# Optimization experiments

Hardware: AMD Instinct MI355X
Metric: run time of the kernel (lower is better)

Reference implementation:

```python
import jax, jax.numpy as jnp
import numpy as np

T, B, L, CTX, H = 512, 512, 16, 64, 128
STATE_DIM, SHOT, PID, DATA = 32, 12, 35, 23


def setup_inputs() -> dict:
    key = jax.random.key(0)
    ks = jax.random.split(key, 64)
    k = iter(ks)
    def rn(shape, s=0.1):
        return (jax.random.normal(next(k), shape) * s).astype(jnp.float32)
    xs = jax.random.normal(next(k), (T, B, DATA), jnp.float32)
    xs = xs.at[:, :, 12].set(jax.random.randint(next(k), (T, B), 0, SHOT).astype(jnp.float32))
    xs = xs.at[:, :, 17].set(jax.random.randint(next(k), (T, B), 0, PID).astype(jnp.float32))
    xs = xs.at[:, :, 20].set(jax.random.randint(next(k), (T, B), 0, SHOT).astype(jnp.float32))
    return dict(
        total_xs=jnp.zeros((1,), jnp.float32),
        xs=xs,
        ts=jnp.linspace(0.0, 2.0, T).astype(jnp.float32),
        noise_std=jnp.asarray(0.1, jnp.float32),
        z0_noise=jax.random.normal(next(k), (B, L), jnp.float32),
        bm_noise=jax.random.normal(next(k), (T - 1, B, L), jnp.float32),
        shot_emb=rn((SHOT, 8)), player_emb=rn((PID, 8)),
        gru_wih=rn((3 * H, STATE_DIM)), gru_whh=rn((3 * H, H)),
        gru_bih=rn((3 * H,)), gru_bhh=rn((3 * H,)),
        enc_w=rn((CTX, H)), enc_b=rn((CTX,)),
        qz0_w=rn((2 * L, CTX)), qz0_b=rn((2 * L,)),
        f_w1=rn((H, L + CTX)), f_b1=rn((H,)), f_w2=rn((H, H)), f_b2=rn((H,)),
        f_w3=rn((L, H)), f_b3=rn((L,)),
        h_w1=rn((H, L)), h_b1=rn((H,)), h_w2=rn((H, H)), h_b2=rn((H,)),
        h_w3=rn((L, H)), h_b3=rn((L,)),
        g_w1=rn((L, H)), g_b1=rn((L, H)), g_w2=rn((L, H)), g_b2=rn((L,)),
        proj_w=rn((STATE_DIM, L)), proj_b=rn((STATE_DIM,)),
        pz0_mean=jnp.zeros((1, L), jnp.float32), pz0_logstd=jnp.zeros((1, L), jnp.float32),
        act_w=rn((128, L)), act_b=rn((128,)),
        act_land_w=rn((2, 128)), act_shot_w=rn((SHOT, 128)), act_move_w=rn((2, 128)),
    )


def _forward(xs, noise_std, shot_emb, player_emb, gru_wih, gru_whh, gru_bih, gru_bhh,
             enc_w, enc_b, qz0_w, qz0_b,
             f_w1, f_b1, f_w2, f_b2, f_w3, f_b3,
             h_w1, h_b1, h_w2, h_b2, h_w3, h_b3,
             g_w1, g_b1, g_w2, g_b2,
             proj_w, proj_b, pz0_mean, pz0_logstd,
             act_w, act_b, act_land_w, act_shot_w, act_move_w,
             ts, z0_noise, bm_noise):
    # --- SDE_embed_and_transform: replace shot/player id cols with embeddings ---
    state = xs[:, :, :18]
    shot_ids = state[:, :, 12].astype(jnp.int32)
    pid_ids = state[:, :, 17].astype(jnp.int32)
    state_t = jnp.concatenate([state[:, :, :12], shot_emb[shot_ids],
                               state[:, :, 13:17], player_emb[pid_ids]], axis=-1)  # (T,B,32)
    xs_t = jnp.concatenate([state_t, xs[:, :, 18:]], axis=-1)  # (T,B,37)
    # --- Encoder: GRU over time-reversed states, linear head, flip back ---
    def gru_step(h, xt):
        gi = xt @ gru_wih.T + gru_bih
        gh = h @ gru_whh.T + gru_bhh
        ir, iz, inn = jnp.split(gi, 3, axis=-1)
        hr, hz, hn = jnp.split(gh, 3, axis=-1)
        r = jax.nn.sigmoid(ir + hr)
        zg = jax.nn.sigmoid(iz + hz)
        n = jnp.tanh(inn + r * hn)
        hnew = (1.0 - zg) * n + zg * h
        return hnew, hnew
    h0 = jnp.zeros((xs.shape[1], gru_whh.shape[1]), xs.dtype)
    _, hs = jax.lax.scan(gru_step, h0, state_t[::-1])
    ctx = (hs @ enc_w.T + enc_b)[::-1]  # (T,B,CTX)
    # --- posterior z0 ---
    qm, qls = jnp.split(ctx[0] @ qz0_w.T + qz0_b, 2, axis=1)
    z0 = qm + jnp.exp(qls) * z0_noise
    # --- Euler-Maruyama with logqp; searchsorted(right) -> ctx[min(i+1,T-1)] = ctx[i+1] ---
    dts = ts[1:] - ts[:-1]  # (T-1,)
    dW = jnp.sqrt(dts)[:, None, None] * bm_noise
    ctx_steps = ctx[1:]
    def mlp3(x, w1, b1, w2, b2, w3, b3):
        h1 = jax.nn.softplus(x @ w1.T + b1)
        h2 = jax.nn.softplus(h1 @ w2.T + b2)
        return h2 @ w3.T + b3
    def g_diag(y):  # (B,L): per-latent-dim scalar nets, batched over L
        hg = jax.nn.softplus(y[:, :, None] * g_w1[None] + g_b1[None])  # (B,L,H)
        return jax.nn.sigmoid(jnp.einsum('blh,lh->bl', hg, g_w2) + g_b2)
    def sde_step(z, inp):
        c, dw, dt = inp
        f_val = mlp3(jnp.concatenate([z, c], axis=1), f_w1, f_b1, f_w2, f_b2, f_w3, f_b3)
        h_val = mlp3(z, h_w1, h_b1, h_w2, h_b2, h_w3, h_b3)
        g_val = g_diag(z)
        u = (f_val - h_val) / g_val
        logr = 0.5 * jnp.sum(u * u, axis=1) * dt
        z_new = z + f_val * dt + g_val * dw
        return z_new, (z_new, logr)
    _, (z_tail, log_ratio) = jax.lax.scan(sde_step, z0, (ctx_steps, dW, dts))
    zs = jnp.concatenate([z0[None], z_tail], axis=0)  # (T,B,L)
    _xs = zs @ proj_w.T + proj_b  # (T,B,32)
    # --- action model losses ---
    a = jax.nn.relu(zs @ act_w.T + act_b)
    land = (a @ act_land_w.T).reshape(-1, 2)
    shot_logits = (a @ act_shot_w.T).reshape(-1, act_shot_w.shape[0])
    move = (a @ act_move_w.T).reshape(-1, 2)
    true_actions = xs_t[:, :, -5:]
    true_land = true_actions[:, :, :2].reshape(-1, 2)
    true_move = true_actions[:, :, 3:].reshape(-1, 2)
    true_shot = true_actions[:, :, 2].astype(jnp.int32).reshape(-1)
    land_loss = jnp.mean((land - true_land) ** 2)
    move_loss = jnp.mean((move - true_move) ** 2)
    logp = jax.nn.log_softmax(shot_logits, axis=-1)
    picked = jnp.take_along_axis(logp, true_shot[:, None], axis=1)[:, 0]
    mask = (true_shot != 0).astype(logp.dtype)  # CrossEntropy ignore_index=0
    shot_loss = -jnp.sum(picked * mask) / jnp.maximum(jnp.sum(mask), 1.0)
    # --- reconstruction log-likelihood ---
    xs_state = xs_t[:, :, :STATE_DIM]
    LOG2PI = 1.8378770664093453
    log_pxs = jnp.mean(jnp.sum(
        -0.5 * ((xs_state - _xs) / noise_std) ** 2 - jnp.log(noise_std) - 0.5 * LOG2PI,
        axis=(0, 2)))
    # --- KL(q(z0) || p(z0)) ---
    var_q = jnp.exp(2.0 * qls)
    var_p = jnp.exp(2.0 * pz0_logstd)
    kl = pz0_logstd - qls + (var_q + (qm - pz0_mean) ** 2) / (2.0 * var_p) - 0.5
    logqp0 = jnp.mean(jnp.sum(kl, axis=1))
    logqp_path = jnp.mean(jnp.sum(log_ratio, axis=0))
    return log_pxs, logqp0 + logqp_path + land_loss + shot_loss + move_loss


def reference(total_xs, xs, ts, noise_std, z0_noise, bm_noise, shot_emb, player_emb,
              gru_wih, gru_whh, gru_bih, gru_bhh, enc_w, enc_b, qz0_w, qz0_b,
              f_w1, f_b1, f_w2, f_b2, f_w3, f_b3, h_w1, h_b1, h_w2, h_b2, h_w3, h_b3,
              g_w1, g_b1, g_w2, g_b2, proj_w, proj_b, pz0_mean, pz0_logstd,
              act_w, act_b, act_land_w, act_shot_w, act_move_w):
    return _forward(xs, noise_std, shot_emb, player_emb, gru_wih, gru_whh, gru_bih, gru_bhh,
                    enc_w, enc_b, qz0_w, qz0_b,
                    f_w1, f_b1, f_w2, f_b2, f_w3, f_b3,
                    h_w1, h_b1, h_w2, h_b2, h_w3, h_b3,
                    g_w1, g_b1, g_w2, g_b2,
                    proj_w, proj_b, pz0_mean, pz0_logstd,
                    act_w, act_b, act_land_w, act_shot_w, act_move_w,
                    ts, z0_noise, bm_noise)
```

## Files before the change

kernel.cpp:

```cpp
#include <hip/hip_runtime.h>
#include <cstdint>

typedef _Float16 f16;
typedef _Float16 f16x2 __attribute__((ext_vector_type(2)));

#define T_STEPS 512
#define B_SZ 512
#define LOG2PI 1.8378770664093453f

__device__ __forceinline__ uint32_t packh2(float a, float b) {
  f16x2 v; v[0] = (f16)a; v[1] = (f16)b;
  return __builtin_bit_cast(uint32_t, v);
}

__device__ __forceinline__ float fdot2(uint32_t a, uint32_t b, float c) {
#if defined(__AMDGCN__) && __has_builtin(__builtin_amdgcn_fdot2)
  return __builtin_amdgcn_fdot2(__builtin_bit_cast(f16x2, a),
                                __builtin_bit_cast(f16x2, b), c, false);
#else
  f16x2 x = __builtin_bit_cast(f16x2, a), y = __builtin_bit_cast(f16x2, b);
  return c + (float)x[0] * (float)y[0] + (float)x[1] * (float)y[1];
#endif
}

#define DOT4(acc, w0, w1, w2, w3, v)                                     \
  do {                                                                   \
    acc = fdot2((w0), (v).x, acc); acc = fdot2((w1), (v).y, acc);        \
    acc = fdot2((w2), (v).z, acc); acc = fdot2((w3), (v).w, acc);        \
  } while (0)

__device__ __forceinline__ float sigmoidf_(float x) {
  return 1.0f / (1.0f + __expf(-x));
}
__device__ __forceinline__ float tanhf_(float x) {
  float ax = fabsf(x);
  float t = __expf(-2.0f * ax);
  float r = (1.0f - t) / (1.0f + t);
  return copysignf(r, x);
}
__device__ __forceinline__ float softplusf_(float x) {
  return fmaxf(x, 0.0f) + __logf(1.0f + __expf(-fabsf(x)));
}

__global__ __launch_bounds__(256) void k_embed(
    const float* __restrict__ xs, const float* __restrict__ shot_emb,
    const float* __restrict__ player_emb, f16* __restrict__ state_t,
    float* __restrict__ accums) {
  if (blockIdx.x == 0 && threadIdx.x < 16) accums[threadIdx.x] = 0.0f;
  size_t idx = (size_t)blockIdx.x * 256 + threadIdx.x;
  const float* xp = xs + idx * 23;
  f16* op = state_t + idx * 32;
  int sid = (int)xp[12];
  int pid = (int)xp[17];
#pragma unroll
  for (int i = 0; i < 12; ++i) op[i] = (f16)xp[i];
  const float* se = shot_emb + sid * 8;
#pragma unroll
  for (int i = 0; i < 8; ++i) op[12 + i] = (f16)se[i];
#pragma unroll
  for (int i = 0; i < 4; ++i) op[20 + i] = (f16)xp[13 + i];
  const float* pe = player_emb + pid * 8;
#pragma unroll
  for (int i = 0; i < 8; ++i) op[24 + i] = (f16)pe[i];
}

__global__ __launch_bounds__(512) void k_gru(
    const f16* __restrict__ state_t, const float* __restrict__ wih,
    const float* __restrict__ whh, const float* __restrict__ bih,
    const float* __restrict__ bhh, const float* __restrict__ enc_w,
    const float* __restrict__ enc_b, const float* __restrict__ qz0_w,
    const float* __restrict__ qz0_b, const float* __restrict__ z0_noise,
    const float* __restrict__ pz0_mean, const float* __restrict__ pz0_logstd,
    f16* __restrict__ ctx, float* __restrict__ z0_out,
    float* __restrict__ accums) {
  __shared__ uint32_t s_x[2][16];
  __shared__ uint32_t s_h[2][64];
  __shared__ float s_gates[2 * 128 * 4];
  __shared__ float s_encp[2 * 64 * 2];
  __shared__ float s_ctx0[2][64];
  __shared__ float s_q[2][32];

  const int tid = threadIdx.x;
  const int bbase = blockIdx.x * 2;
  const uint32_t* stu = (const uint32_t*)state_t;

  uint32_t wA[64];
  uint32_t wB[16];
  float bias0 = 0.f, bias1 = 0.f, encbr = 0.f;

  if (tid < 256) {
    int g = tid >> 7, du = tid & 127;
    const float* whr = whh + (size_t)(g * 128 + du) * 128;
#pragma unroll
    for (int i = 0; i < 64; ++i) wA[i] = packh2(whr[2 * i], whr[2 * i + 1]);
    const float* wxr = wih + (size_t)(g * 128 + du) * 32;
#pragma unroll
    for (int i = 0; i < 16; ++i) wB[i] = packh2(wxr[2 * i], wxr[2 * i + 1]);
    bias0 = bih[g * 128 + du] + bhh[g * 128 + du];
  } else if (tid < 384) {
    int du = tid - 256;
    const float* whr = whh + (size_t)(256 + du) * 128;
#pragma unroll
    for (int i = 0; i < 64; ++i) wA[i] = packh2(whr[2 * i], whr[2 * i + 1]);
    const float* wxr = wih + (size_t)(256 + du) * 32;
#pragma unroll
    for (int i = 0; i < 16; ++i) wB[i] = packh2(wxr[2 * i], wxr[2 * i + 1]);
    bias0 = bih[256 + du];
    bias1 = bhh[256 + du];
  } else {
    int e = tid - 384, c = e & 63, ks = e >> 6;
    const float* wer = enc_w + (size_t)c * 128 + ks * 64;
#pragma unroll
    for (int i = 0; i < 32; ++i) wA[i] = packh2(wer[2 * i], wer[2 * i + 1]);
    encbr = enc_b[c];
  }

  if (tid < 128) s_h[tid >> 6][tid & 63] = 0u;
  if (tid < 32) {
    int b = tid >> 4, i = tid & 15;
    s_x[b][i] = stu[((size_t)(T_STEPS - 1) * B_SZ + bbase + b) * 16 + i];
  }
  float h_old = 0.0f;
  __syncthreads();

  for (int t = T_STEPS - 1; t >= 0; --t) {
    uint4 xpref = make_uint4(0, 0, 0, 0);
    if (tid < 256) {
      int g = tid >> 7, du = tid & 127;
#pragma unroll
      for (int b = 0; b < 2; ++b) {
        float a = bias0;
        const uint4* xq = (const uint4*)&s_x[b][0];
#pragma unroll
        for (int j = 0; j < 4; ++j) {
          uint4 v = xq[j];
          DOT4(a, wB[4 * j], wB[4 * j + 1], wB[4 * j + 2], wB[4 * j + 3], v);
        }
        const uint4* hq = (const uint4*)&s_h[b][0];
#pragma unroll
        for (int j = 0; j < 16; ++j) {
          uint4 v = hq[j];
          DOT4(a, wA[4 * j], wA[4 * j + 1], wA[4 * j + 2], wA[4 * j + 3], v);
        }
        s_gates[(b * 128 + du) * 4 + g] = a;
      }
    } else if (tid < 384) {
      int du = tid - 256;
#pragma unroll
      for (int b = 0; b < 2; ++b) {
        float aI = bias0, aH = bias1;
        const uint4* xq = (const uint4*)&s_x[b][0];
#pragma unroll
        for (int j = 0; j < 4; ++j) {
          uint4 v = xq[j];
          DOT4(aI, wB[4 * j], wB[4 * j + 1], wB[4 * j + 2], wB[4 * j + 3], v);
        }
        const uint4* hq = (const uint4*)&s_h[b][0];
#pragma unroll
        for (int j = 0; j < 16; ++j) {
          uint4 v = hq[j];
          DOT4(aH, wA[4 * j], wA[4 * j + 1], wA[4 * j + 2], wA[4 * j + 3], v);
        }
        s_gates[(b * 128 + du) * 4 + 2] = aI;
        s_gates[(b * 128 + du) * 4 + 3] = aH;
      }
    } else {
      int e = tid - 384, ks = e >> 6, cc = e & 63;
      (void)cc;
      if (t < T_STEPS - 1) {
#pragma unroll
        for (int b = 0; b < 2; ++b) {
          float a = 0.f;
          const uint4* hq = (const uint4*)&s_h[b][ks * 32];
#pragma unroll
          for (int j = 0; j < 8; ++j) {
            uint4 v = hq[j];
            DOT4(a, wA[4 * j], wA[4 * j + 1], wA[4 * j + 2], wA[4 * j + 3], v);
          }
          s_encp[(b * 64 + cc) * 2 + ks] = a;
        }
      }
      if (e < 8 && t > 0) {
        int b = e & 1, q = e >> 1;
        xpref = *(const uint4*)(stu +
                                ((size_t)(t - 1) * B_SZ + bbase + b) * 16 + q * 4);
      }
    }
    __syncthreads();
    if (tid < 256) {
      int b = tid >> 7, du = tid & 127;
      const float4 gt = *(const float4*)&s_gates[(b * 128 + du) * 4];
      float r = sigmoidf_(gt.x), zg = sigmoidf_(gt.y);
      float n = tanhf_(gt.z + r * gt.w);
      float hnew = (1.0f - zg) * n + zg * h_old;
      h_old = hnew;
      ((f16*)&s_h[b][0])[du] = (f16)hnew;
    } else if (tid >= 384) {
      int e = tid - 384, cc = e & 63, b = e >> 6;
      if (t < T_STEPS - 1) {
        float2 p = *(const float2*)&s_encp[(b * 64 + cc) * 2];
        ctx[((size_t)(t + 1) * B_SZ + bbase + b) * 64 + cc] =
            (f16)(p.x + p.y + encbr);
      }
      if (e < 8 && t > 0) {
        int b2 = e & 1, q = e >> 1;
        *(uint4*)&s_x[b2][q * 4] = xpref;
      }
    }
    __syncthreads();
  }

  if (tid >= 384) {
    int e = tid - 384, ks = e >> 6, cc = e & 63;
#pragma unroll
    for (int b = 0; b < 2; ++b) {
      float a = 0.f;
      const uint4* hq = (const uint4*)&s_h[b][ks * 32];
#pragma unroll
      for (int j = 0; j < 8; ++j) {
        uint4 v = hq[j];
        DOT4(a, wA[4 * j], wA[4 * j + 1], wA[4 * j + 2], wA[4 * j + 3], v);
      }
      s_encp[(b * 64 + cc) * 2 + ks] = a;
    }
  }
  __syncthreads();
  if (tid >= 384) {
    int e = tid - 384, cc = e & 63, b = e >> 6;
    float2 p = *(const float2*)&s_encp[(b * 64 + cc) * 2];
    float val = p.x + p.y + encbr;
    ctx[((size_t)bbase + b) * 64 + cc] = (f16)val;
    s_ctx0[b][cc] = val;
  }
  __syncthreads();
  if (tid < 64) {
    int b = tid >> 5, o = tid & 31;
    float acc = qz0_b[o];
#pragma unroll 8
    for (int k = 0; k < 64; ++k) acc += qz0_w[o * 64 + k] * s_ctx0[b][k];
    s_q[b][o] = acc;
  }
  __syncthreads();
  if (tid < 32) {
    int b = tid >> 4, l = tid & 15;
    int bg = bbase + b;
    float qm = s_q[b][l], qls = s_q[b][16 + l];
    float z0v = qm + __expf(qls) * z0_noise[bg * 16 + l];
    z0_out[bg * 16 + l] = z0v;
    float pm = pz0_mean[l], pls = pz0_logstd[l];
    float var_q = __expf(2.0f * qls);
    float var_p = __expf(2.0f * pls);
    float dm = qm - pm;
    float kl = pls - qls + (var_q + dm * dm) / (2.0f * var_p) - 0.5f;
    atomicAdd(&accums[5], kl);
  }
}

__global__ __launch_bounds__(512) void k_sde(
    const f16* __restrict__ ctx, const float* __restrict__ z0_in,
    const float* __restrict__ ts, const float* __restrict__ bm_noise,
    const float* __restrict__ fw1, const float* __restrict__ fb1,
    const float* __restrict__ fw2, const float* __restrict__ fb2,
    const float* __restrict__ fw3, const float* __restrict__ fb3,
    const float* __restrict__ hw1, const float* __restrict__ hb1,
    const float* __restrict__ hw2, const float* __restrict__ hb2,
    const float* __restrict__ hw3, const float* __restrict__ hb3,
    const float* __restrict__ gw1, const float* __restrict__ gb1,
    const float* __restrict__ gw2, const float* __restrict__ gb2,
    f16* __restrict__ zs, float* __restrict__ accums) {
  __shared__ uint32_t s_x2[2][40];
  __shared__ float s_zf[2][16];
  __shared__ uint32_t s_h1[2][2][64];
  __shared__ uint32_t s_h2[2][2][64];
  __shared__ float s_gp[256];
  __shared__ float s_gv[32];
  __shared__ float s_p2[2 * 2 * 128 * 2];
  __shared__ float s_p3[2 * 2 * 16 * 8];
  __shared__ float s_dts[512];

  const int tid = threadIdx.x;
  const int bbase = blockIdx.x * 2;

  uint32_t uw[48];
  uint32_t wP2[32];
  uint32_t wP3[8];
  float bias1r = 0.f, bias2r = 0.f, gb2r = 0.f, fb3r = 0.f, hb3r = 0.f;

  if (tid < 256) {
    int l = tid & 15, k8 = (tid >> 4) & 7;
#pragma unroll
    for (int i = 0; i < 16; ++i) {
      int h = k8 * 16 + i;
      uw[i] = __builtin_bit_cast(uint32_t, gw1[l * 128 + h]);
      uw[16 + i] = __builtin_bit_cast(uint32_t, gb1[l * 128 + h]);
      uw[32 + i] = __builtin_bit_cast(uint32_t, gw2[l * 128 + h]);
    }
  } else if (tid < 384) {
    int u = tid - 256;
    const float* w = fw1 + (size_t)u * 80;
#pragma unroll
    for (int i = 0; i < 40; ++i) uw[i] = packh2(w[2 * i], w[2 * i + 1]);
    bias1r = fb1[u];
  } else {
    int u = tid - 384;
    const float* w = hw1 + (size_t)u * 16;
#pragma unroll
    for (int i = 0; i < 8; ++i) uw[i] = packh2(w[2 * i], w[2 * i + 1]);
    bias1r = hb1[u];
  }
  {
    int u = tid & 127, ks = (tid >> 7) & 1, mlp = tid >> 8;
    const float* w = (mlp ? hw2 : fw2) + (size_t)u * 128 + ks * 64;
#pragma unroll
    for (int i = 0; i < 32; ++i) wP2[i] = packh2(w[2 * i], w[2 * i + 1]);
    bias2r = (mlp ? hb2 : fb2)[u];
  }
  if (tid < 128 || (tid >= 256 && tid < 384)) {
    int o = tid & 15, k8 = (tid >> 4) & 7;
    const float* w = ((tid >= 256) ? hw3 : fw3) + (size_t)o * 128 + k8 * 16;
#pragma unroll
    for (int i = 0; i < 8; ++i) wP3[i] = packh2(w[2 * i], w[2 * i + 1]);
  }
  if (tid >= 128 && tid < 160) gb2r = gb2[tid & 15];
  if (tid < 32) {
    fb3r = fb3[tid & 15];
    hb3r = hb3[tid & 15];
  }

  if (tid < 511) s_dts[tid] = ts[tid + 1] - ts[tid];
  float bmc = 0.f;
  uint4 cpref = make_uint4(0, 0, 0, 0);
  if (tid < 32) {
    int b = tid >> 4, l = tid & 15, bg = bbase + b;
    float z = z0_in[bg * 16 + l];
    s_zf[b][l] = z;
    ((f16*)&s_x2[b][0])[l] = (f16)z;
    zs[(size_t)bg * 16 + l] = (f16)z;
    bmc = bm_noise[((size_t)0 * B_SZ + bg) * 16 + l];
  }
  if (tid >= 32 && tid < 48) {
    int i = tid - 32, b = i & 1, q = i >> 1;
    const uint32_t* cu = (const uint32_t*)ctx;
    uint4 v = *(const uint4*)(cu + ((size_t)1 * B_SZ + bbase + b) * 32 + q * 4);
    *(uint4*)&s_x2[b][8 + q * 4] = v;
  }
  float path_acc = 0.0f;
  __syncthreads();

  for (int t = 0; t < T_STEPS - 1; ++t) {
    float bmn = 0.f;
    if (tid < 32 && t < T_STEPS - 2) {
      int b = tid >> 4, l = tid & 15, bg = bbase + b;
      bmn = bm_noise[((size_t)(t + 1) * B_SZ + bg) * 16 + l];
    }
    if (tid >= 32 && tid < 48 && t <= T_STEPS - 3) {
      int i = tid - 32, b = i & 1, q = i >> 1;
      const uint32_t* cu = (const uint32_t*)ctx;
      cpref = *(const uint4*)(cu +
                              ((size_t)(t + 2) * B_SZ + bbase + b) * 32 + q * 4);
    }
    if (tid < 256) {
      int b = tid >> 7, l = tid & 15, k8 = (tid >> 4) & 7;
      float y = s_zf[b][l];
      float acc = 0.f;
#pragma unroll
      for (int i = 0; i < 16; ++i) {
        float pre = fmaf(y, __builtin_bit_cast(float, uw[i]),
                         __builtin_bit_cast(float, uw[16 + i]));
        acc = fmaf(softplusf_(pre), __builtin_bit_cast(float, uw[32 + i]), acc);
      }
      s_gp[(b * 16 + l) * 8 + k8] = acc;
    } else if (tid < 384) {
      int u = tid - 256;
#pragma unroll
      for (int b = 0; b < 2; ++b) {
        float a = bias1r;
        const uint4* xq = (const uint4*)&s_x2[b][0];
#pragma unroll
        for (int j = 0; j < 10; ++j) {
          uint4 v = xq[j];
          DOT4(a, uw[4 * j], uw[4 * j + 1], uw[4 * j + 2], uw[4 * j + 3], v);
        }
        ((f16*)&s_h1[0][b][0])[u] = (f16)softplusf_(a);
      }
    } else {
      int u = tid - 384;
#pragma unroll
      for (int b = 0; b < 2; ++b) {
        float a = bias1r;
        const uint4* xq = (const uint4*)&s_x2[b][0];
#pragma unroll
        for (int j = 0; j < 2; ++j) {
          uint4 v = xq[j];
          DOT4(a, uw[4 * j], uw[4 * j + 1], uw[4 * j + 2], uw[4 * j + 3], v);
        }
        ((f16*)&s_h1[1][b][0])[u] = (f16)softplusf_(a);
      }
    }
    __syncthreads();
    {
      int u = tid & 127, ks = (tid >> 7) & 1, mlp = tid >> 8;
#pragma unroll
      for (int b = 0; b < 2; ++b) {
        float a = 0.f;
        const uint4* hq = (const uint4*)&s_h1[mlp][b][ks * 32];
#pragma unroll
        for (int j = 0; j < 8; ++j) {
          uint4 v = hq[j];
          DOT4(a, wP2[4 * j], wP2[4 * j + 1], wP2[4 * j + 2], wP2[4 * j + 3], v);
        }
        s_p2[((mlp * 2 + b) * 128 + u) * 2 + ks] = a;
      }
    }
    __syncthreads();
    {
      int u = tid & 127, b = (tid >> 7) & 1, mlp = tid >> 8;
      float2 p = *(const float2*)&s_p2[((mlp * 2 + b) * 128 + u) * 2];
      ((f16*)&s_h2[mlp][b][0])[u] = (f16)softplusf_(p.x + p.y + bias2r);
    }
    __syncthreads();
    if (tid < 128 || (tid >= 256 && tid < 384)) {
      int o = tid & 15, k8 = (tid >> 4) & 7, mlp = tid >> 8;
#pragma unroll
      for (int b = 0; b < 2; ++b) {
        float a = 0.f;
        const uint4* hq = (const uint4*)&s_h2[mlp][b][k8 * 8];
#pragma unroll
        for (int j = 0; j < 2; ++j) {
          uint4 v = hq[j];
          DOT4(a, wP3[4 * j], wP3[4 * j + 1], wP3[4 * j + 2], wP3[4 * j + 3], v);
        }
        s_p3[((mlp * 2 + b) * 16 + o) * 8 + k8] = a;
      }
    } else if (tid >= 128 && tid < 160) {
      int i = tid - 128, b = i >> 4, l = i & 15;
      const float4* gp = (const float4*)&s_gp[(b * 16 + l) * 8];
      float4 g0 = gp[0], g1 = gp[1];
      float sum = g0.x + g0.y + g0.z + g0.w + g1.x + g1.y + g1.z + g1.w + gb2r;
      s_gv[b * 16 + l] = sigmoidf_(sum);
    }
    __syncthreads();
    if (tid < 32) {
      int b = tid >> 4, l = tid & 15, bg = bbase + b;
      const float4* fp = (const float4*)&s_p3[((0 * 2 + b) * 16 + l) * 8];
      const float4* hp = (const float4*)&s_p3[((2 + b) * 16 + l) * 8];
      float4 f0 = fp[0], f1v = fp[1], h0 = hp[0], h1v = hp[1];
      float fv = fb3r + f0.x + f0.y + f0.z + f0.w + f1v.x + f1v.y + f1v.z + f1v.w;
      float hv = hb3r + h0.x + h0.y + h0.z + h0.w + h1v.x + h1v.y + h1v.z + h1v.w;
      float gv = s_gv[b * 16 + l];
      float dt = s_dts[t];
      float u = (fv - hv) / gv;
      float lsum = u * u;
      lsum += __shfl_xor(lsum, 1);
      lsum += __shfl_xor(lsum, 2);
      lsum += __shfl_xor(lsum, 4);
      lsum += __shfl_xor(lsum, 8);
      if (l == 0) path_acc += 0.5f * lsum * dt;
      float dw = sqrtf(dt) * bmc;
      float zn = s_zf[b][l] + fv * dt + gv * dw;
      s_zf[b][l] = zn;
      ((f16*)&s_x2[b][0])[l] = (f16)zn;
      zs[((size_t)(t + 1) * B_SZ + bg) * 16 + l] = (f16)zn;
      bmc = bmn;
    } else if (tid >= 32 && tid < 48 && t <= T_STEPS - 3) {
      int i = tid - 32, b = i & 1, q = i >> 1;
      *(uint4*)&s_x2[b][8 + q * 4] = cpref;
    }
    __syncthreads();
  }
  if (tid < 32 && (tid & 15) == 0) atomicAdd(&accums[6], path_acc);
}

__global__ __launch_bounds__(256) void k_dec(
    const f16* __restrict__ zs, const f16* __restrict__ state_t,
    const float* __restrict__ xs, const float* __restrict__ proj_w,
    const float* __restrict__ proj_b, const float* __restrict__ act_w,
    const float* __restrict__ act_b, const float* __restrict__ land_w,
    const float* __restrict__ shot_w, const float* __restrict__ move_w,
    float* __restrict__ accums) {
  __shared__ uint32_t s_proj[8 * 32];
  __shared__ uint32_t s_act[8 * 128];
  __shared__ uint32_t s_head[128 * 8];
  __shared__ float s_pb[32], s_ab[128];
  __shared__ float s_red[4 * 5];

  const int tid = threadIdx.x;
  for (int id = tid; id < 8 * 32; id += 256) {
    int kp = id & 7, n = id >> 3;
    s_proj[kp * 32 + n] = packh2(proj_w[n * 16 + 2 * kp], proj_w[n * 16 + 2 * kp + 1]);
  }
  for (int id = tid; id < 8 * 128; id += 256) {
    int kp = id & 7, n = id >> 3;
    s_act[kp * 128 + n] = packh2(act_w[n * 16 + 2 * kp], act_w[n * 16 + 2 * kp + 1]);
  }
  for (int id = tid; id < 128 * 8; id += 256) {
    int j = id >> 3, p = id & 7;
    int h0 = 2 * p, h1 = 2 * p + 1;
    float w0 = (h0 < 2) ? land_w[h0 * 128 + j]
                        : (h0 < 14 ? shot_w[(h0 - 2) * 128 + j]
                                   : move_w[(h0 - 14) * 128 + j]);
    float w1 = (h1 < 2) ? land_w[h1 * 128 + j]
                        : (h1 < 14 ? shot_w[(h1 - 2) * 128 + j]
                                   : move_w[(h1 - 14) * 128 + j]);
    s_head[j * 8 + p] = packh2(w0, w1);
  }
  if (tid < 32) s_pb[tid] = proj_b[tid];
  if (tid < 128) s_ab[tid] = act_b[tid];
  __syncthreads();

  size_t idx = (size_t)blockIdx.x * 256 + tid;
  uint32_t z2[8];
  const uint32_t* zp = (const uint32_t*)(zs + idx * 16);
#pragma unroll
  for (int i = 0; i < 8; ++i) z2[i] = zp[i];
  uint32_t stv[16];
  const uint32_t* stp = (const uint32_t*)(state_t + idx * 32);
#pragma unroll
  for (int i = 0; i < 16; ++i) stv[i] = stp[i];

  float sqsum = 0.0f;
#pragma unroll 4
  for (int i = 0; i < 32; ++i) {
    float acc = s_pb[i];
#pragma unroll
    for (int kp = 0; kp < 8; ++kp) acc = fdot2(s_proj[kp * 32 + i], z2[kp], acc);
    f16x2 sv = __builtin_bit_cast(f16x2, stv[i >> 1]);
    float d = (float)sv[i & 1] - acc;
    sqsum += d * d;
  }

  float hd[16];
#pragma unroll
  for (int i = 0; i < 16; ++i) hd[i] = 0.0f;
#pragma unroll 2
  for (int j = 0; j < 128; ++j) {
    float a = s_ab[j];
#pragma unroll
    for (int kp = 0; kp < 8; ++kp) a = fdot2(s_act[kp * 128 + j], z2[kp], a);
    a = fmaxf(a, 0.0f);
#pragma unroll
    for (int p = 0; p < 8; ++p) {
      f16x2 w = __builtin_bit_cast(f16x2, s_head[j * 8 + p]);
      hd[2 * p] += (float)w[0] * a;
      hd[2 * p + 1] += (float)w[1] * a;
    }
  }
  const float* xp = xs + idx * 23;
  float dl0 = hd[0] - xp[18], dl1 = hd[1] - xp[19];
  float land = dl0 * dl0 + dl1 * dl1;
  float dm0 = hd[14] - xp[21], dm1 = hd[15] - xp[22];
  float move = dm0 * dm0 + dm1 * dm1;
  int sid = (int)xp[20];
  float m = hd[2];
#pragma unroll
  for (int s = 1; s < 12; ++s) m = fmaxf(m, hd[2 + s]);
  float sume = 0.0f;
#pragma unroll
  for (int s = 0; s < 12; ++s) sume += __expf(hd[2 + s] - m);
  float lse = m + __logf(sume);
  float pl = 0.0f;
#pragma unroll
  for (int s = 0; s < 12; ++s)
    if (s == sid) pl = hd[2 + s];
  float picked = 0.0f, cnt = 0.0f;
  if (sid != 0) {
    picked = pl - lse;
    cnt = 1.0f;
  }
  float vals[5] = {sqsum, land, move, picked, cnt};
#pragma unroll
  for (int v = 0; v < 5; ++v) {
    float x = vals[v];
    for (int off = 1; off < 64; off <<= 1) x += __shfl_xor(x, off);
    vals[v] = x;
  }
  int lane = tid & 63, wv = tid >> 6;
  if (lane == 0) {
#pragma unroll
    for (int v = 0; v < 5; ++v) s_red[wv * 5 + v] = vals[v];
  }
  __syncthreads();
  if (tid == 0) {
#pragma unroll
    for (int v = 0; v < 5; ++v) {
      float s = s_red[v] + s_red[5 + v] + s_red[10 + v] + s_red[15 + v];
      atomicAdd(&accums[v], s);
    }
  }
}

__global__ void k_fin(const float* __restrict__ accums,
                      const float* __restrict__ noise_std,
                      float* __restrict__ out) {
  if (threadIdx.x == 0 && blockIdx.x == 0) {
    float sd = noise_std[0];
    float log_pxs = -0.5f * accums[0] / (sd * sd * (float)B_SZ) -
                    (float)T_STEPS * 32.0f * (logf(sd) + 0.5f * LOG2PI);
    float land = accums[1] / (float)(T_STEPS * B_SZ * 2);
    float move = accums[2] / (float)(T_STEPS * B_SZ * 2);
    float shot = -accums[3] / fmaxf(accums[4], 1.0f);
    float out1 = accums[5] / (float)B_SZ + accums[6] / (float)B_SZ + land + shot + move;
    out[0] = log_pxs;
    out[1] = out1;
  }
}

extern "C" void kernel_launch(void* const* d_in, const int* in_sizes, int n_in,
                              void* d_out, int out_size, void* d_ws,
                              size_t ws_size, hipStream_t stream) {
  const float* xs = (const float*)d_in[1];
  const float* ts = (const float*)d_in[2];
  const float* noise_std = (const float*)d_in[3];
  const float* z0_noise = (const float*)d_in[4];
  const float* bm_noise = (const float*)d_in[5];
  const float* shot_emb = (const float*)d_in[6];
  const float* player_emb = (const float*)d_in[7];
  const float* gru_wih = (const float*)d_in[8];
  const float* gru_whh = (const float*)d_in[9];
  const float* gru_bih = (const float*)d_in[10];
  const float* gru_bhh = (const float*)d_in[11];
  const float* enc_w = (const float*)d_in[12];
  const float* enc_b = (const float*)d_in[13];
  const float* qz0_w = (const float*)d_in[14];
  const float* qz0_b = (const float*)d_in[15];
  const float* f_w1 = (const float*)d_in[16];
  const float* f_b1 = (const float*)d_in[17];
  const float* f_w2 = (const float*)d_in[18];
  const float* f_b2 = (const float*)d_in[19];
  const float* f_w3 = (const float*)d_in[20];
  const float* f_b3 = (const float*)d_in[21];
  const float* h_w1 = (const float*)d_in[22];
  const float* h_b1 = (const float*)d_in[23];
  const float* h_w2 = (const float*)d_in[24];
  const float* h_b2 = (const float*)d_in[25];
  const float* h_w3 = (const float*)d_in[26];
  const float* h_b3 = (const float*)d_in[27];
  const float* g_w1 = (const float*)d_in[28];
  const float* g_b1 = (const float*)d_in[29];
  const float* g_w2 = (const float*)d_in[30];
  const float* g_b2 = (const float*)d_in[31];
  const float* proj_w = (const float*)d_in[32];
  const float* proj_b = (const float*)d_in[33];
  const float* pz0_mean = (const float*)d_in[34];
  const float* pz0_logstd = (const float*)d_in[35];
  const float* act_w = (const float*)d_in[36];
  const float* act_b = (const float*)d_in[37];
  const float* act_land_w = (const float*)d_in[38];
  const float* act_shot_w = (const float*)d_in[39];
  const float* act_move_w = (const float*)d_in[40];

  char* ws = (char*)d_ws;
  float* accums = (float*)ws;
  f16* state_t = (f16*)(ws + 256);
  f16* ctx = (f16*)(ws + 256 + 16777216);
  float* z0b = (float*)(ws + 256 + 16777216 + 33554432);
  f16* zs = (f16*)(ws + 256 + 16777216 + 33554432 + 32768);

  k_embed<<<1024, 256, 0, stream>>>(xs, shot_emb, player_emb, state_t, accums);
  k_gru<<<256, 512, 0, stream>>>(state_t, gru_wih, gru_whh, gru_bih, gru_bhh,
                                 enc_w, enc_b, qz0_w, qz0_b, z0_noise, pz0_mean,
                                 pz0_logstd, ctx, z0b, accums);
  k_sde<<<256, 512, 0, stream>>>(ctx, z0b, ts, bm_noise, f_w1, f_b1, f_w2, f_b2,
                                 f_w3, f_b3, h_w1, h_b1, h_w2, h_b2, h_w3, h_b3,
                                 g_w1, g_b1, g_w2, g_b2, zs, accums);
  k_dec<<<1024, 256, 0, stream>>>(zs, state_t, xs, proj_w, proj_b, act_w, act_b,
                                  act_land_w, act_shot_w, act_move_w, accums);
  k_fin<<<1, 64, 0, stream>>>(accums, noise_std, (float*)d_out);
}
```

Measured before the change: 1.996 ms.

## Reduce SDE step barriers via shuffle reductions and fused output-layer epilogue

Reassigns thread mappings in the per-timestep SDE loop so the split-K partial sums of the second layer are combined with lane shuffles instead of a shared-memory pass. The third layer and the drift/diffusion update are merged into one phase using shuffles, which removes the s_p2, s_p3 and s_gv buffers and two __syncthreads per step. Dot-product loops also gain split accumulators to shorten dependency chains. The cost is more registers per thread (larger wP3) and concentrating the final-layer work on 128 threads.

```diff
diff --git a/kernel.cpp b/kernel.cpp
--- a/kernel.cpp
+++ b/kernel.cpp
@@ -273,9 +273,6 @@
   __shared__ uint32_t s_h1[2][2][64];
   __shared__ uint32_t s_h2[2][2][64];
   __shared__ float s_gp[256];
-  __shared__ float s_gv[32];
-  __shared__ float s_p2[2 * 2 * 128 * 2];
-  __shared__ float s_p3[2 * 2 * 16 * 8];
   __shared__ float s_dts[512];
 
   const int tid = threadIdx.x;
@@ -283,7 +280,7 @@
 
   uint32_t uw[48];
   uint32_t wP2[32];
-  uint32_t wP3[8];
+  uint32_t wP3[32];
   float bias1r = 0.f, bias2r = 0.f, gb2r = 0.f, fb3r = 0.f, hb3r = 0.f;
 
   if (tid < 256) {
@@ -309,52 +306,52 @@
     bias1r = hb1[u];
   }
   {
-    int u = tid & 127, ks = (tid >> 7) & 1, mlp = tid >> 8;
+    int u = (tid >> 1) & 127, ks = tid & 1, mlp = tid >> 8;
     const float* w = (mlp ? hw2 : fw2) + (size_t)u * 128 + ks * 64;
 #pragma unroll
     for (int i = 0; i < 32; ++i) wP2[i] = packh2(w[2 * i], w[2 * i + 1]);
     bias2r = (mlp ? hb2 : fb2)[u];
   }
-  if (tid < 128 || (tid >= 256 && tid < 384)) {
-    int o = tid & 15, k8 = (tid >> 4) & 7;
-    const float* w = ((tid >= 256) ? hw3 : fw3) + (size_t)o * 128 + k8 * 16;
-#pragma unroll
-    for (int i = 0; i < 8; ++i) wP3[i] = packh2(w[2 * i], w[2 * i + 1]);
-  }
-  if (tid >= 128 && tid < 160) gb2r = gb2[tid & 15];
-  if (tid < 32) {
-    fb3r = fb3[tid & 15];
-    hb3r = hb3[tid & 15];
+  if (tid < 128) {
+    int l = (tid >> 2) & 15, mlp = (tid >> 1) & 1, kh = tid & 1;
+    const float* w = (mlp ? hw3 : fw3) + (size_t)l * 128 + kh * 64;
+#pragma unroll
+    for (int i = 0; i < 32; ++i) wP3[i] = packh2(w[2 * i], w[2 * i + 1]);
+    if ((tid & 3) == 0) {
+      gb2r = gb2[l];
+      fb3r = fb3[l];
+      hb3r = hb3[l];
+    }
   }
 
   if (tid < 511) s_dts[tid] = ts[tid + 1] - ts[tid];
   float bmc = 0.f;
+  float path_acc = 0.0f;
   uint4 cpref = make_uint4(0, 0, 0, 0);
-  if (tid < 32) {
-    int b = tid >> 4, l = tid & 15, bg = bbase + b;
+  if (tid < 128 && (tid & 3) == 0) {
+    int b = tid >> 6, l = (tid >> 2) & 15, bg = bbase + b;
     float z = z0_in[bg * 16 + l];
     s_zf[b][l] = z;
     ((f16*)&s_x2[b][0])[l] = (f16)z;
     zs[(size_t)bg * 16 + l] = (f16)z;
     bmc = bm_noise[((size_t)0 * B_SZ + bg) * 16 + l];
   }
-  if (tid >= 32 && tid < 48) {
-    int i = tid - 32, b = i & 1, q = i >> 1;
+  if (tid >= 128 && tid < 144) {
+    int i = tid - 128, b = i & 1, q = i >> 1;
     const uint32_t* cu = (const uint32_t*)ctx;
     uint4 v = *(const uint4*)(cu + ((size_t)1 * B_SZ + bbase + b) * 32 + q * 4);
     *(uint4*)&s_x2[b][8 + q * 4] = v;
   }
-  float path_acc = 0.0f;
   __syncthreads();
 
   for (int t = 0; t < T_STEPS - 1; ++t) {
     float bmn = 0.f;
-    if (tid < 32 && t < T_STEPS - 2) {
-      int b = tid >> 4, l = tid & 15, bg = bbase + b;
-      bmn = bm_noise[((size_t)(t + 1) * B_SZ + bg) * 16 + l];
-    }
-    if (tid >= 32 && tid < 48 && t <= T_STEPS - 3) {
-      int i = tid - 32, b = i & 1, q = i >> 1;
+    if (tid < 128 && (tid & 3) == 0 && t < T_STEPS - 2) {
+      int b = tid >> 6, l = (tid >> 2) & 15;
+      bmn = bm_noise[((size_t)(t + 1) * B_SZ + bbase + b) * 16 + l];
+    }
+    if (tid >= 128 && tid < 144 && t <= T_STEPS - 3) {
+      int i = tid - 128, b = i & 1, q = i >> 1;
       const uint32_t* cu = (const uint32_t*)ctx;
       cpref = *(const uint4*)(cu +
                               ((size_t)(t + 2) * B_SZ + bbase + b) * 32 + q * 4);
@@ -374,14 +371,15 @@
       int u = tid - 256;
 #pragma unroll
       for (int b = 0; b < 2; ++b) {
-        float a = bias1r;
+        float a0 = bias1r, a1 = 0.f;
         const uint4* xq = (const uint4*)&s_x2[b][0];
 #pragma unroll
-        for (int j = 0; j < 10; ++j) {
-          uint4 v = xq[j];
-          DOT4(a, uw[4 * j], uw[4 * j + 1], uw[4 * j + 2], uw[4 * j + 3], v);
+        for (int j = 0; j < 10; j += 2) {
+          uint4 v0 = xq[j], v1 = xq[j + 1];
+          DOT4(a0, uw[4 * j], uw[4 * j + 1], uw[4 * j + 2], uw[4 * j + 3], v0);
+          DOT4(a1, uw[4 * j + 4], uw[4 * j + 5], uw[4 * j + 6], uw[4 * j + 7], v1);
         }
-        ((f16*)&s_h1[0][b][0])[u] = (f16)softplusf_(a);
+        ((f16*)&s_h1[0][b][0])[u] = (f16)softplusf_(a0 + a1);
       }
     } else {
       int u = tid - 384;
@@ -399,76 +397,68 @@
     }
     __syncthreads();
     {
-      int u = tid & 127, ks = (tid >> 7) & 1, mlp = tid >> 8;
-#pragma unroll
-      for (int b = 0; b < 2; ++b) {
-        float a = 0.f;
-        const uint4* hq = (const uint4*)&s_h1[mlp][b][ks * 32];
-#pragma unroll
-        for (int j = 0; j < 8; ++j) {
-          uint4 v = hq[j];
-          DOT4(a, wP2[4 * j], wP2[4 * j + 1], wP2[4 * j + 2], wP2[4 * j + 3], v);
-        }
-        s_p2[((mlp * 2 + b) * 128 + u) * 2 + ks] = a;
-      }
+      int u = (tid >> 1) & 127, ks = tid & 1, mlp = tid >> 8;
+      float p0a = 0.f, p0b = 0.f, p1a = 0.f, p1b = 0.f;
+      const uint4* h0q = (const uint4*)&s_h1[mlp][0][ks * 32];
+      const uint4* h1q = (const uint4*)&s_h1[mlp][1][ks * 32];
+#pragma unroll
+      for (int j = 0; j < 8; j += 2) {
+        uint4 v0 = h0q[j], v1 = h0q[j + 1];
+        DOT4(p0a, wP2[4 * j], wP2[4 * j + 1], wP2[4 * j + 2], wP2[4 * j + 3], v0);
+        DOT4(p0b, wP2[4 * j + 4], wP2[4 * j + 5], wP2[4 * j + 6], wP2[4 * j + 7], v1);
+        uint4 w0 = h1q[j], w1 = h1q[j + 1];
+        DOT4(p1a, wP2[4 * j], wP2[4 * j + 1], wP2[4 * j + 2], wP2[4 * j + 3], w0);
+        DOT4(p1b, wP2[4 * j + 4], wP2[4 * j + 5], wP2[4 * j + 6], wP2[4 * j + 7], w1);
+      }
+      float p0 = p0a + p0b, p1 = p1a + p1b;
+      p0 += __shfl_xor(p0, 1);
+      p1 += __shfl_xor(p1, 1);
+      float sel = ks ? p1 : p0;
+      ((f16*)&s_h2[mlp][ks][0])[u] = (f16)softplusf_(sel + bias2r);
     }
     __syncthreads();
-    {
-      int u = tid & 127, b = (tid >> 7) & 1, mlp = tid >> 8;
-      float2 p = *(const float2*)&s_p2[((mlp * 2 + b) * 128 + u) * 2];
-      ((f16*)&s_h2[mlp][b][0])[u] = (f16)softplusf_(p.x + p.y + bias2r);
+    if (tid < 128) {
+      int b = tid >> 6, l = (tid >> 2) & 15, mlp = (tid >> 1) & 1, kh = tid & 1;
+      const uint4* hq = (const uint4*)&s_h2[mlp][b][kh * 32];
+      float a0 = 0.f, a1 = 0.f;
+#pragma unroll
+      for (int j = 0; j < 8; j += 2) {
+        uint4 v0 = hq[j], v1 = hq[j + 1];
+        DOT4(a0, wP3[4 * j], wP3[4 * j + 1], wP3[4 * j + 2], wP3[4 * j + 3], v0);
+        DOT4(a1, wP3[4 * j + 4], wP3[4 * j + 5], wP3[4 * j + 6], wP3[4 * j + 7], v1);
+      }
+      float a = a0 + a1;
+      float full = a + __shfl_xor(a, 1);
+      float other = __shfl_xor(full, 2);
+      if ((tid & 3) == 0) {
+        float fv = full + fb3r;
+        float hv = other + hb3r;
+        const float4* gp = (const float4*)&s_gp[(b * 16 + l) * 8];
+        float4 g0 = gp[0], g1 = gp[1];
+        float gv = sigmoidf_(g0.x + g0.y + g0.z + g0.w +
+                             g1.x + g1.y + g1.z + g1.w + gb2r);
+        float dt = s_dts[t];
+        float u_ = (fv - hv) / gv;
+        float lsum = u_ * u_;
+        lsum += __shfl_xor(lsum, 4);
+        lsum += __shfl_xor(lsum, 8);
+        lsum += __shfl_xor(lsum, 16);
+        lsum += __shfl_xor(lsum, 32);
+        if (l == 0) path_acc += 0.5f * lsum * dt;
+        float dw = sqrtf(dt) * bmc;
+        float zn = s_zf[b][l] + fv * dt + gv * dw;
+        s_zf[b][l] = zn;
+        ((f16*)&s_x2[b][0])[l] = (f16)zn;
+        zs[((size_t)(t + 1) * B_SZ + bbase + b) * 16 + l] = (f16)zn;
+        bmc = bmn;
+      }
+    } else if (tid >= 128 && tid < 144 && t <= T_STEPS - 3) {
+      int i = tid - 128, b = i & 1, q = i >> 1;
+      *(uint4*)&s_x2[b][8 + q * 4] = cpref;
     }
     __syncthreads();
-    if (tid < 128 || (tid >= 256 && tid < 384)) {
-      int o = tid & 15, k8 = (tid >> 4) & 7, mlp = tid >> 8;
-#pragma unroll
-      for (int b = 0; b < 2; ++b) {
-        float a = 0.f;
-        const uint4* hq = (const uint4*)&s_h2[mlp][b][k8 * 8];
-#pragma unroll
-        for (int j = 0; j < 2; ++j) {
-          uint4 v = hq[j];
-          DOT4(a, wP3[4 * j], wP3[4 * j + 1], wP3[4 * j + 2], wP3[4 * j + 3], v);
-        }
-        s_p3[((mlp * 2 + b) * 16 + o) * 8 + k8] = a;
-      }
-    } else if (tid >= 128 && tid < 160) {
-      int i = tid - 128, b = i >> 4, l = i & 15;
-      const float4* gp = (const float4*)&s_gp[(b * 16 + l) * 8];
-      float4 g0 = gp[0], g1 = gp[1];
-      float sum = g0.x + g0.y + g0.z + g0.w + g1.x + g1.y + g1.z + g1.w + gb2r;
-      s_gv[b * 16 + l] = sigmoidf_(sum);
-    }
-    __syncthreads();
-    if (tid < 32) {
-      int b = tid >> 4, l = tid & 15, bg = bbase + b;
-      const float4* fp = (const float4*)&s_p3[((0 * 2 + b) * 16 + l) * 8];
-      const float4* hp = (const float4*)&s_p3[((2 + b) * 16 + l) * 8];
-      float4 f0 = fp[0], f1v = fp[1], h0 = hp[0], h1v = hp[1];
-      float fv = fb3r + f0.x + f0.y + f0.z + f0.w + f1v.x + f1v.y + f1v.z + f1v.w;
-      float hv = hb3r + h0.x + h0.y + h0.z + h0.w + h1v.x + h1v.y + h1v.z + h1v.w;
-      float gv = s_gv[b * 16 + l];
-      float dt = s_dts[t];
-      float u = (fv - hv) / gv;
-      float lsum = u * u;
-      lsum += __shfl_xor(lsum, 1);
-      lsum += __shfl_xor(lsum, 2);
-      lsum += __shfl_xor(lsum, 4);
-      lsum += __shfl_xor(lsum, 8);
-      if (l == 0) path_acc += 0.5f * lsum * dt;
-      float dw = sqrtf(dt) * bmc;
-      float zn = s_zf[b][l] + fv * dt + gv * dw;
-      s_zf[b][l] = zn;
-      ((f16*)&s_x2[b][0])[l] = (f16)zn;
-      zs[((size_t)(t + 1) * B_SZ + bg) * 16 + l] = (f16)zn;
-      bmc = bmn;
-    } else if (tid >= 32 && tid < 48 && t <= T_STEPS - 3) {
-      int i = tid - 32, b = i & 1, q = i >> 1;
-      *(uint4*)&s_x2[b][8 + q * 4] = cpref;
-    }
-    __syncthreads();
-  }
-  if (tid < 32 && (tid & 15) == 0) atomicAdd(&accums[6], path_acc);
+  }
+  if (tid == 0 || tid == 64) atomicAdd(&accums[6], path_acc);
 }
 
 __global__ __launch_bounds__(256) void k_dec(
```

Result: no change. 1.986 ms (-0.5%).
